# Optimization experiments

Measured on AMD Instinct MI355X. Metric: run time of the kernel, lower is better.

The kernel has to match this reference:

```python
import jax, jax.numpy as jnp
import numpy as np

DIM = 768
NUM_HEADS = 12
HEAD_DIM = DIM // NUM_HEADS
SCALE = HEAD_DIM ** -0.5
B, N = 8, 1024


def setup_inputs() -> dict:
    key = jax.random.key(0)
    k1, k2, k3, k4 = jax.random.split(key, 4)
    s = 1.0 / np.sqrt(DIM)
    return {
        "x": jax.random.normal(k1, (B, N, DIM), dtype=jnp.float32),
        "w_qkv": jax.random.normal(k2, (DIM, 3 * DIM), dtype=jnp.float32) * s,  # qkv_bias=False
        "w_proj": jax.random.normal(k3, (DIM, DIM), dtype=jnp.float32) * s,
        "b_proj": jax.random.normal(k4, (DIM,), dtype=jnp.float32) * 0.01,
    }


def reference(x, w_qkv, w_proj, b_proj):
    Bb, Nn, C = x.shape
    qkv = x @ w_qkv  # [B, N, 3C]
    qkv = qkv.reshape(Bb, Nn, 3, NUM_HEADS, HEAD_DIM)
    q = qkv[:, :, 0].transpose(0, 2, 1, 3)  # [B, H, N, d]
    k = qkv[:, :, 1].transpose(0, 2, 1, 3)
    v = qkv[:, :, 2].transpose(0, 2, 1, 3)
    attn = jnp.einsum("bhqd,bhkd->bhqk", q, k) * SCALE
    attn = jax.nn.softmax(attn, axis=-1)  # dropout p=0 -> identity
    out = jnp.einsum("bhqk,bhkd->bhqd", attn, v)
    out = out.transpose(0, 2, 1, 3).reshape(Bb, Nn, C)
    return out @ w_proj + b_proj
```

## Files before the change

### kernel.cpp

```cpp
#include <hip/hip_runtime.h>
#include <stdint.h>

typedef __attribute__((ext_vector_type(8))) __bf16 bf16x8;
typedef __attribute__((ext_vector_type(8))) unsigned short u16x8;
typedef __attribute__((ext_vector_type(4))) unsigned short u16x4;
typedef __attribute__((ext_vector_type(4))) short s16x4;
typedef __attribute__((ext_vector_type(4))) float f32x4;

typedef unsigned int u32_as1 __attribute__((address_space(1)));
typedef unsigned int u32_as3 __attribute__((address_space(3)));

__device__ __forceinline__ unsigned short f2bf(float f) {
  unsigned int u = __float_as_uint(f);
  u += 0x7fffu + ((u >> 16) & 1u);
  return (unsigned short)(u >> 16);
}

__device__ __forceinline__ bf16x8 ld_frag(const unsigned short* p) {
  return __builtin_bit_cast(bf16x8, *(const u16x8*)p);
}

__device__ __forceinline__ f32x4 mfma16(s16x4 a, s16x4 b, f32x4 c) {
#if __has_builtin(__builtin_amdgcn_mfma_f32_16x16x16bf16_1k)
  return __builtin_amdgcn_mfma_f32_16x16x16bf16_1k(a, b, c, 0, 0, 0);
#elif __has_builtin(__builtin_amdgcn_mfma_f32_16x16x16_bf16_1k)
  return __builtin_amdgcn_mfma_f32_16x16x16_bf16_1k(a, b, c, 0, 0, 0);
#else
  asm volatile("v_mfma_f32_16x16x16_bf16 %0, %1, %2, %0"
               : "+v"(c) : "v"(a), "v"(b));
  return c;
#endif
}

__device__ __forceinline__ float fast_exp2(float x) {
#if __has_builtin(__builtin_amdgcn_exp2f)
  return __builtin_amdgcn_exp2f(x);
#else
  return exp2f(x);
#endif
}

__device__ __forceinline__ void async16(const void* g, void* l) {
  const u32_as1* gp = (const u32_as1*)(uintptr_t)g;
  u32_as3* lp = (u32_as3*)(uintptr_t)l;
  __builtin_amdgcn_global_load_lds(gp, lp, 16, 0, 0);
}

template <int N> __device__ __forceinline__ void wait_vmcnt() {
  if constexpr (N == 0)      asm volatile("s_waitcnt vmcnt(0)" ::: "memory");
  else if constexpr (N == 2) asm volatile("s_waitcnt vmcnt(2)" ::: "memory");
  else if constexpr (N == 3) asm volatile("s_waitcnt vmcnt(3)" ::: "memory");
  else if constexpr (N == 4) asm volatile("s_waitcnt vmcnt(4)" ::: "memory");
  else if constexpr (N == 6) asm volatile("s_waitcnt vmcnt(6)" ::: "memory");
  else if constexpr (N == 8) asm volatile("s_waitcnt vmcnt(8)" ::: "memory");
}

__global__ __launch_bounds__(256) void prep_kernel(
    const float* __restrict__ x, const float* __restrict__ w_qkv,
    const float* __restrict__ w_proj, u16x4* __restrict__ x_bf,
    unsigned short* __restrict__ wqkvT, unsigned short* __restrict__ wprojT) {
  const int bid = blockIdx.x;
  const int t = threadIdx.x;
  if (bid < 6144) {
    const int i = bid * 256 + t;
    float4 v = ((const float4*)x)[i];
    u16x4 o;
    o[0] = f2bf(v.x); o[1] = f2bf(v.y); o[2] = f2bf(v.z); o[3] = f2bf(v.w);
    x_bf[i] = o;
    return;
  }
  __shared__ float tile[32][33];
  const float* w; unsigned short* wt; int N, bx, by;
  if (bid < 6144 + 1728) { const int r = bid - 6144; w = w_qkv; wt = wqkvT; N = 2304; bx = r % 72; by = r / 72; }
  else                   { const int r = bid - 7872; w = w_proj; wt = wprojT; N = 768; bx = r % 24; by = r / 24; }
  const int n0 = bx * 32, k0 = by * 32;
  const int tx = t & 31, ty = t >> 5;
#pragma unroll
  for (int r = 0; r < 4; r++)
    tile[ty + r * 8][tx] = w[(k0 + ty + r * 8) * N + n0 + tx];
  __syncthreads();
#pragma unroll
  for (int r = 0; r < 4; r++)
    wt[(n0 + ty + r * 8) * 768 + k0 + tx] = f2bf(tile[tx][ty + r * 8]);
}

template <int EPI, int NT, int NBLK, int MINW>
__global__ __launch_bounds__(256, MINW) void gemm_bt(
    const unsigned short* __restrict__ A, const unsigned short* __restrict__ Bt,
    unsigned short* __restrict__ qb, unsigned short* __restrict__ kb,
    unsigned short* __restrict__ vtb, float* __restrict__ outp,
    const float* __restrict__ bias) {
  constexpr int STAGE = 4096 + NT * 2048;
  constexpr int NK = 24;
  constexpr int NLD = 2 + NT;
  __shared__ unsigned short smem[3 * STAGE];

  const int t = threadIdx.x;
  const int lane = t & 63, w = t >> 6;
  const int quad = lane >> 4, l15 = lane & 15;

  const int bid = blockIdx.x;
  const int xcd = bid & 7, slot = bid >> 3;
  const int m0 = (xcd * 8 + slot / NBLK) * 128;
  const int n0 = (slot % NBLK) * (NT * 64);
  const int wm = (w & 1) * 64, wn = (w >> 1) * (NT * 32);

  f32x4 acc[4][NT * 2];
  const f32x4 fzero = {0.f, 0.f, 0.f, 0.f};
#pragma unroll
  for (int i = 0; i < 4; i++)
#pragma unroll
    for (int j = 0; j < NT * 2; j++) acc[i][j] = fzero;

  const int srow = w * 16 + (lane >> 2);
  const int scol = (((lane & 3) - (srow >> 1)) & 3) * 8;
  const unsigned short* Ag = A + (m0 + srow) * 768 + scol;
  const unsigned short* Bg = Bt + (n0 + srow) * 768 + scol;
  const int ldso = w * 512 + lane * 8;

  auto fill = [&](int k, int stg) {
    unsigned short* As = smem + stg * STAGE;
    async16(Ag + k * 32, As + ldso);
    async16(Ag + 64 * 768 + k * 32, As + ldso + 2048);
#pragma unroll
    for (int f = 0; f < NT; f++)
      async16(Bg + f * 64 * 768 + k * 32, As + 4096 + ldso + f * 2048);
  };

  fill(0, 0);
  fill(1, 1);

#pragma unroll
  for (int k = 0; k < NK; ++k) {
    if (k + 1 < NK) wait_vmcnt<NLD>();
    else            wait_vmcnt<0>();
    asm volatile("s_barrier" ::: "memory");
    if (k + 2 < NK) fill(k + 2, (k + 2) % 3);

    const unsigned short* As = smem + (k % 3) * STAGE;
    const unsigned short* Bs = As + 4096;

    bf16x8 af[4], bfr[NT * 2];
#pragma unroll
    for (int i = 0; i < 4; i++) {
      const int row = wm + i * 16 + l15;
      af[i] = ld_frag(As + row * 32 + (((quad + (row >> 1)) & 3) << 3));
    }
#pragma unroll
    for (int j = 0; j < NT * 2; j++) {
      const int row = wn + j * 16 + l15;
      bfr[j] = ld_frag(Bs + row * 32 + (((quad + (row >> 1)) & 3) << 3));
    }
#pragma unroll
    for (int i = 0; i < 4; i++)
#pragma unroll
      for (int j = 0; j < NT * 2; j++)
        acc[i][j] = __builtin_amdgcn_mfma_f32_16x16x32_bf16(af[i], bfr[j], acc[i][j], 0, 0, 0);
  }

#pragma unroll
  for (int i = 0; i < 4; i++) {
    const int gmb = m0 + wm + i * 16 + quad * 4;
#pragma unroll
    for (int j = 0; j < NT * 2; j++) {
      const int gc = n0 + wn + j * 16 + l15;
#pragma unroll
      for (int r = 0; r < 4; r++) {
        const int gm = gmb + r;
        float v = acc[i][j][r];
        if (EPI == 0) {
          const int b = gm >> 10, tok = gm & 1023;
          const int which = (gc >= 1536) ? 2 : (gc >= 768 ? 1 : 0);
          const int rem = gc - which * 768;
          const int h = rem >> 6, d = rem & 63;
          const int bh = b * 12 + h;
          const unsigned short bv = f2bf(v);
          if (which == 0)      qb[(bh << 16) + (tok << 6) + d] = bv;
          else if (which == 1) kb[(bh << 16) + (tok << 6) + d] = bv;
          else                 vtb[(bh << 16) + (d << 10) + tok] = bv;
        } else {
          outp[gm * 768 + gc] = v + bias[gc];
        }
      }
    }
  }
}

#define SWZC(row, c) (((row) << 6) + ((((c) + (row)) & 7) << 3))
#define C2 0.1803368801111244f

__global__ __launch_bounds__(256, 3) void attn_kernel(
    const unsigned short* __restrict__ qb, const unsigned short* __restrict__ kb,
    const unsigned short* __restrict__ vtb, unsigned short* __restrict__ aout) {
  __shared__ unsigned short smem[3 * 8192];

  const int t = threadIdx.x;
  const int lane = t & 63, w = t >> 6;
  const int quad = lane >> 4, l15 = lane & 15;
  const int bh = blockIdx.x;
  const int b = bh / 12, h = bh - b * 12;
  const int q0 = blockIdx.y * 128;
  const int base = bh << 16;

  bf16x8 qf[2][2];
#pragma unroll
  for (int qt = 0; qt < 2; qt++)
#pragma unroll
    for (int s = 0; s < 2; s++)
      qf[qt][s] = ld_frag(qb + base + ((q0 + w * 32 + qt * 16 + l15) << 6) +
                          s * 32 + quad * 8);

  f32x4 oacc[4][2];
  const f32x4 fzero = {0.f, 0.f, 0.f, 0.f};
#pragma unroll
  for (int dt = 0; dt < 4; dt++) { oacc[dt][0] = fzero; oacc[dt][1] = fzero; }
  float lsum0 = 0.f, lsum1 = 0.f;

  const int srow = t >> 3, schk = t & 7;
  const int c0 = ((schk - srow) & 7) * 8;
  const int c1 = ((schk - (srow + 32)) & 7) * 8;

  auto fillkv = [&](int tile, int buf) {
    const int kv0 = tile * 64;
    unsigned short* Ks = smem + buf * 8192;
    unsigned short* Vts = Ks + 4096;
    async16(kb + base + ((kv0 + srow) << 6) + c0, Ks + t * 8);
    async16(kb + base + ((kv0 + srow + 32) << 6) + c1, Ks + 2048 + t * 8);
    async16(vtb + base + (srow << 10) + kv0 + c0, Vts + t * 8);
    async16(vtb + base + ((srow + 32) << 10) + kv0 + c1, Vts + 2048 + t * 8);
  };

  fillkv(0, 0);
  fillkv(1, 1);
  int cur = 0;
  for (int it = 0; it < 16; ++it) {
    if (it < 15) wait_vmcnt<4>(); else wait_vmcnt<0>();
    asm volatile("s_barrier" ::: "memory");
    if (it + 2 < 16) {
      int tgt = cur + 2; if (tgt >= 3) tgt -= 3;
      fillkv(it + 2, tgt);
    }
    const unsigned short* Ks = smem + cur * 8192;
    const unsigned short* Vts = Ks + 4096;

    f32x4 st[4][2];
#pragma unroll
    for (int tc = 0; tc < 4; tc++) { st[tc][0] = fzero; st[tc][1] = fzero; }
#pragma unroll
    for (int s = 0; s < 2; s++) {
#pragma unroll
      for (int tc = 0; tc < 4; tc++) {
        const bf16x8 kf = ld_frag(Ks + SWZC(tc * 16 + l15, s * 4 + quad));
        st[tc][0] = __builtin_amdgcn_mfma_f32_16x16x32_bf16(kf, qf[0][s], st[tc][0], 0, 0, 0);
        st[tc][1] = __builtin_amdgcn_mfma_f32_16x16x32_bf16(kf, qf[1][s], st[tc][1], 0, 0, 0);
      }
    }

    s16x4 pf[4][2];
#pragma unroll
    for (int tc = 0; tc < 4; tc++) {
#pragma unroll
      for (int qt = 0; qt < 2; qt++) {
        const float p0 = fast_exp2(st[tc][qt][0] * C2);
        const float p1 = fast_exp2(st[tc][qt][1] * C2);
        const float p2 = fast_exp2(st[tc][qt][2] * C2);
        const float p3 = fast_exp2(st[tc][qt][3] * C2);
        const float ps = (p0 + p1) + (p2 + p3);
        if (qt == 0) lsum0 += ps; else lsum1 += ps;
        s16x4 pk;
        pk[0] = (short)f2bf(p0); pk[1] = (short)f2bf(p1);
        pk[2] = (short)f2bf(p2); pk[3] = (short)f2bf(p3);
        pf[tc][qt] = pk;
      }
    }

#pragma unroll
    for (int tc = 0; tc < 4; tc++) {
#pragma unroll
      for (int dt = 0; dt < 4; dt++) {
        const int row = dt * 16 + l15;
        const int addr = (row << 6) + ((((tc * 2 + (quad >> 1)) + row) & 7) << 3) +
                         ((quad & 1) << 2);
        const s16x4 vf = *(const s16x4*)(Vts + addr);
        oacc[dt][0] = mfma16(vf, pf[tc][0], oacc[dt][0]);
        oacc[dt][1] = mfma16(vf, pf[tc][1], oacc[dt][1]);
      }
    }

    cur += 1; if (cur == 3) cur = 0;
  }

  lsum0 += __shfl_xor(lsum0, 16); lsum0 += __shfl_xor(lsum0, 32);
  lsum1 += __shfl_xor(lsum1, 16); lsum1 += __shfl_xor(lsum1, 32);
  const float inv0 = 1.f / lsum0, inv1 = 1.f / lsum1;

  __syncthreads();
  unsigned short* Ot = smem;
#pragma unroll
  for (int dt = 0; dt < 4; dt++) {
#pragma unroll
    for (int qt = 0; qt < 2; qt++) {
      const float inv = qt == 0 ? inv0 : inv1;
      const int qrow = (w * 32 + qt * 16 + l15) * 72 + dt * 16 + quad * 4;
#pragma unroll
      for (int r = 0; r < 4; r++)
        Ot[qrow + r] = f2bf(oacc[dt][qt][r] * inv);
    }
  }
  __syncthreads();
#pragma unroll
  for (int it = 0; it < 4; it++) {
    const int q = it * 32 + (t >> 3);
    const int d0 = (t & 7) * 8;
    const u16x8 v = *(const u16x8*)(Ot + q * 72 + d0);
    *(u16x8*)(aout + (b * 1024 + q0 + q) * 768 + h * 64 + d0) = v;
  }
}

extern "C" void kernel_launch(void* const* d_in, const int* in_sizes, int n_in,
                              void* d_out, int out_size, void* d_ws, size_t ws_size,
                              hipStream_t stream) {
  (void)in_sizes; (void)n_in; (void)out_size; (void)ws_size;
  const float* x = (const float*)d_in[0];
  const float* w_qkv = (const float*)d_in[1];
  const float* w_proj = (const float*)d_in[2];
  const float* b_proj = (const float*)d_in[3];
  float* out = (float*)d_out;

  char* ws = (char*)d_ws;
  unsigned short* x_bf   = (unsigned short*)(ws);
  unsigned short* wqkvT  = (unsigned short*)(ws + 12582912);
  unsigned short* wprojT = (unsigned short*)(ws + 16121856);
  unsigned short* qb     = (unsigned short*)(ws + 17301504);
  unsigned short* kb     = (unsigned short*)(ws + 29884416);
  unsigned short* vtb    = (unsigned short*)(ws + 42467328);
  unsigned short* aout   = x_bf;

  prep_kernel<<<8448, 256, 0, stream>>>(x, w_qkv, w_proj, (u16x4*)x_bf, wqkvT, wprojT);
  gemm_bt<0, 2, 18, 3><<<1152, 256, 0, stream>>>(x_bf, wqkvT, qb, kb, vtb, nullptr, nullptr);
  attn_kernel<<<dim3(96, 8), 256, 0, stream>>>(qb, kb, vtb, aout);
  gemm_bt<1, 1, 12, 4><<<768, 256, 0, stream>>>(aout, wprojT, nullptr, nullptr, nullptr, out, b_proj);
}
```

Baseline: 194.5 us.

## Rewrite GEMMs as 256x128 tiles with 512 threads and split-phase pipelining

Replaces the templated 128xN GEMM with a 256x128-tile kernel using 8 waves, K-tiles of 64, XOR-swizzled LDS layout, and a three-stage async pipeline whose loads are split into two phases interleaved with MFMA work. It also raises wave priority around the MFMA block. The larger tiles are meant to improve operand reuse and cut global/LDS traffic per flop. In exchange it uses more LDS and fewer blocks, especially 192 blocks for the projection GEMM, which may underfill the GPU's CUs.

Measured after the change: 184.8 us. -5.0%, faster.

```diff
diff --git a/kernel.cpp b/kernel.cpp
--- a/kernel.cpp
+++ b/kernel.cpp
@@ -48,11 +48,8 @@
 
 template <int N> __device__ __forceinline__ void wait_vmcnt() {
   if constexpr (N == 0)      asm volatile("s_waitcnt vmcnt(0)" ::: "memory");
-  else if constexpr (N == 2) asm volatile("s_waitcnt vmcnt(2)" ::: "memory");
-  else if constexpr (N == 3) asm volatile("s_waitcnt vmcnt(3)" ::: "memory");
   else if constexpr (N == 4) asm volatile("s_waitcnt vmcnt(4)" ::: "memory");
   else if constexpr (N == 6) asm volatile("s_waitcnt vmcnt(6)" ::: "memory");
-  else if constexpr (N == 8) asm volatile("s_waitcnt vmcnt(8)" ::: "memory");
 }
 
 __global__ __launch_bounds__(256) void prep_kernel(
@@ -84,86 +81,108 @@
     wt[(n0 + ty + r * 8) * 768 + k0 + tx] = f2bf(tile[tx][ty + r * 8]);
 }
 
-template <int EPI, int NT, int NBLK, int MINW>
-__global__ __launch_bounds__(256, MINW) void gemm_bt(
+template <int EPI>
+__global__ __launch_bounds__(512, 2) void gemm256(
     const unsigned short* __restrict__ A, const unsigned short* __restrict__ Bt,
     unsigned short* __restrict__ qb, unsigned short* __restrict__ kb,
     unsigned short* __restrict__ vtb, float* __restrict__ outp,
     const float* __restrict__ bias) {
-  constexpr int STAGE = 4096 + NT * 2048;
-  constexpr int NK = 24;
-  constexpr int NLD = 2 + NT;
-  __shared__ unsigned short smem[3 * STAGE];
+  constexpr int NKT = 12;
+  constexpr int SSH = 24576;
+  __shared__ unsigned short smem[3 * SSH];
 
   const int t = threadIdx.x;
   const int lane = t & 63, w = t >> 6;
   const int quad = lane >> 4, l15 = lane & 15;
+  const int wm = w >> 1, wn = w & 1;
 
   const int bid = blockIdx.x;
   const int xcd = bid & 7, slot = bid >> 3;
-  const int m0 = (xcd * 8 + slot / NBLK) * 128;
-  const int n0 = (slot % NBLK) * (NT * 64);
-  const int wm = (w & 1) * 64, wn = (w >> 1) * (NT * 32);
-
-  f32x4 acc[4][NT * 2];
+  const int m0 = (xcd * 4 + (slot & 3)) * 256;
+  const int n0 = (slot >> 2) * 128;
+
+  int aoff[4][2], boff[4][2];
+#pragma unroll
+  for (int i = 0; i < 4; i++) {
+    const int row = wm * 64 + i * 16 + l15;
+    const int rs = row & 7;
+#pragma unroll
+    for (int kk = 0; kk < 2; kk++)
+      aoff[i][kk] = row * 64 + (((kk * 4 + quad) ^ rs) << 3);
+  }
+#pragma unroll
+  for (int j = 0; j < 4; j++) {
+    const int row = wn * 64 + j * 16 + l15;
+    const int rs = row & 7;
+#pragma unroll
+    for (int kk = 0; kk < 2; kk++)
+      boff[j][kk] = 16384 + row * 64 + (((kk * 4 + quad) ^ rs) << 3);
+  }
+
+  const int srow = t >> 3;
+  const int gch = ((t & 7) ^ (srow & 7)) << 3;
+  const unsigned short* Ags = A + (m0 + srow) * 768 + gch;
+  const unsigned short* Bgs = Bt + (n0 + srow) * 768 + gch;
+
+  f32x4 acc[4][4];
   const f32x4 fzero = {0.f, 0.f, 0.f, 0.f};
 #pragma unroll
   for (int i = 0; i < 4; i++)
 #pragma unroll
-    for (int j = 0; j < NT * 2; j++) acc[i][j] = fzero;
-
-  const int srow = w * 16 + (lane >> 2);
-  const int scol = (((lane & 3) - (srow >> 1)) & 3) * 8;
-  const unsigned short* Ag = A + (m0 + srow) * 768 + scol;
-  const unsigned short* Bg = Bt + (n0 + srow) * 768 + scol;
-  const int ldso = w * 512 + lane * 8;
-
-  auto fill = [&](int k, int stg) {
-    unsigned short* As = smem + stg * STAGE;
-    async16(Ag + k * 32, As + ldso);
-    async16(Ag + 64 * 768 + k * 32, As + ldso + 2048);
-#pragma unroll
-    for (int f = 0; f < NT; f++)
-      async16(Bg + f * 64 * 768 + k * 32, As + 4096 + ldso + f * 2048);
+    for (int j = 0; j < 4; j++) acc[i][j] = fzero;
+
+  auto stage = [&](int kt, int part) {
+    unsigned short* s = smem + (kt % 3) * SSH + t * 8;
+    const int ko = kt * 64;
+    if (part == 0) {
+      async16(Ags + ko, s);
+      async16(Ags + 49152 + ko, s + 4096);
+      async16(Ags + 98304 + ko, s + 8192);
+    } else {
+      async16(Ags + 147456 + ko, s + 12288);
+      async16(Bgs + ko, s + 16384);
+      async16(Bgs + 49152 + ko, s + 20480);
+    }
   };
 
-  fill(0, 0);
-  fill(1, 1);
-
-#pragma unroll
-  for (int k = 0; k < NK; ++k) {
-    if (k + 1 < NK) wait_vmcnt<NLD>();
-    else            wait_vmcnt<0>();
-    asm volatile("s_barrier" ::: "memory");
-    if (k + 2 < NK) fill(k + 2, (k + 2) % 3);
-
-    const unsigned short* As = smem + (k % 3) * STAGE;
-    const unsigned short* Bs = As + 4096;
-
-    bf16x8 af[4], bfr[NT * 2];
-#pragma unroll
-    for (int i = 0; i < 4; i++) {
-      const int row = wm + i * 16 + l15;
-      af[i] = ld_frag(As + row * 32 + (((quad + (row >> 1)) & 3) << 3));
-    }
-#pragma unroll
-    for (int j = 0; j < NT * 2; j++) {
-      const int row = wn + j * 16 + l15;
-      bfr[j] = ld_frag(Bs + row * 32 + (((quad + (row >> 1)) & 3) << 3));
-    }
-#pragma unroll
-    for (int i = 0; i < 4; i++)
-#pragma unroll
-      for (int j = 0; j < NT * 2; j++)
-        acc[i][j] = __builtin_amdgcn_mfma_f32_16x16x32_bf16(af[i], bfr[j], acc[i][j], 0, 0, 0);
+  stage(0, 0); stage(0, 1);
+  stage(1, 0); stage(1, 1);
+
+#pragma unroll
+  for (int kt = 0; kt < NKT; ++kt) {
+    const unsigned short* S = smem + (kt % 3) * SSH;
+#pragma unroll
+    for (int ph = 0; ph < 2; ++ph) {
+      if (ph == 0) {
+        if (kt < NKT - 1) wait_vmcnt<6>();
+        else              wait_vmcnt<0>();
+      }
+      __builtin_amdgcn_s_barrier();
+
+      bf16x8 af[4], bf[4];
+#pragma unroll
+      for (int i = 0; i < 4; i++) af[i] = ld_frag(S + aoff[i][ph]);
+#pragma unroll
+      for (int j = 0; j < 4; j++) bf[j] = ld_frag(S + boff[j][ph]);
+
+      if (kt + 2 < NKT) stage(kt + 2, ph);
+
+      __builtin_amdgcn_s_setprio(1);
+#pragma unroll
+      for (int i = 0; i < 4; i++)
+#pragma unroll
+        for (int j = 0; j < 4; j++)
+          acc[i][j] = __builtin_amdgcn_mfma_f32_16x16x32_bf16(af[i], bf[j], acc[i][j], 0, 0, 0);
+      __builtin_amdgcn_s_setprio(0);
+    }
   }
 
 #pragma unroll
   for (int i = 0; i < 4; i++) {
-    const int gmb = m0 + wm + i * 16 + quad * 4;
-#pragma unroll
-    for (int j = 0; j < NT * 2; j++) {
-      const int gc = n0 + wn + j * 16 + l15;
+    const int gmb = m0 + wm * 64 + i * 16 + quad * 4;
+#pragma unroll
+    for (int j = 0; j < 4; j++) {
+      const int gc = n0 + wn * 64 + j * 16 + l15;
 #pragma unroll
       for (int r = 0; r < 4; r++) {
         const int gm = gmb + r;
@@ -337,7 +356,7 @@
   unsigned short* aout   = x_bf;
 
   prep_kernel<<<8448, 256, 0, stream>>>(x, w_qkv, w_proj, (u16x4*)x_bf, wqkvT, wprojT);
-  gemm_bt<0, 2, 18, 3><<<1152, 256, 0, stream>>>(x_bf, wqkvT, qb, kb, vtb, nullptr, nullptr);
+  gemm256<0><<<576, 512, 0, stream>>>(x_bf, wqkvT, qb, kb, vtb, nullptr, nullptr);
   attn_kernel<<<dim3(96, 8), 256, 0, stream>>>(qb, kb, vtb, aout);
-  gemm_bt<1, 1, 12, 4><<<768, 256, 0, stream>>>(aout, wprojT, nullptr, nullptr, nullptr, out, b_proj);
-}
+  gemm256<1><<<192, 512, 0, stream>>>(aout, wprojT, nullptr, nullptr, nullptr, out, b_proj);
+}
```
